# Optimization experiments

Measured on AMD Instinct MI355X. Metric: run time of the kernel, lower is better.

## Reference

```python
import jax, jax.numpy as jnp
import numpy as np

NUM_HEADS = 8


def setup_inputs() -> dict:
    key = jax.random.key(0)
    k0, k1, k2 = jax.random.split(key, 3)
    B, C, D, H, W = 2, 256, 16, 16, 8
    x = jax.random.normal(k0, (B, C, D, H, W), dtype=jnp.float32)
    # 1x1x1 Conv3d weights are pointwise linear maps over channels
    w_qkv = jax.random.normal(k1, (3 * C, C), dtype=jnp.float32) * 0.02
    b_qkv = jnp.zeros((3 * C,), dtype=jnp.float32)
    w_out = jax.random.normal(k2, (C, C), dtype=jnp.float32) * 0.02
    b_out = jnp.zeros((C,), dtype=jnp.float32)
    return {"x": x, "w_qkv": w_qkv, "b_qkv": b_qkv, "w_out": w_out, "b_out": b_out}


def reference(x, w_qkv, b_qkv, w_out, b_out):
    b, c, d, h, w = x.shape
    nh = NUM_HEADS
    hd = c // nh
    scale = hd ** (-0.5)
    n = d * h * w
    xf = x.reshape(b, c, n)  # flatten spatial volume to N tokens
    # to_qkv: pointwise conv == channel-mixing matmul
    qkv = jnp.einsum('oc,bcn->bon', w_qkv, xf) + b_qkv[None, :, None]
    # torch: view(b, H, 3*hd, N) then chunk(3, dim=2) -> per-head channel grouping
    qkv = qkv.reshape(b, nh, 3 * hd, n)
    q, k, v = jnp.split(qkv, 3, axis=2)  # each (b, nh, hd, n)
    sim = jnp.einsum('bhcn,bhcm->bhnm', q, k) * scale  # (b, nh, N, N)
    attn = jax.nn.softmax(sim, axis=-1)
    out = jnp.einsum('bhnm,bhcm->bhcn', attn, v)  # (b, nh, hd, N)
    out = out.reshape(b, c, n)
    out = jnp.einsum('oc,bcn->bon', w_out, out) + b_out[None, :, None]
    return x + out.reshape(b, c, d, h, w)
```

## Files before the change

kernel.cpp:

```cpp
#include <hip/hip_runtime.h>
#include <hip/hip_bf16.h>
#include <math.h>

#define BB 2
#define CC 256
#define NH 8
#define HD 32
#define NN 2048
#define QBLK 64
#define QK_SCALE 0.25500917f

typedef __attribute__((ext_vector_type(8))) short short8;
typedef __attribute__((ext_vector_type(8))) unsigned short ushort8;
typedef __attribute__((ext_vector_type(4))) float f32x4;

__device__ inline unsigned short f2bf(float f) {
    __hip_bfloat16 h = __float2bfloat16(f);
    return __builtin_bit_cast(unsigned short, h);
}
__device__ inline int xcd_chunk(int orig, int nwg) {
    int q = nwg >> 3, r = nwg & 7, x = orig & 7, s = orig >> 3;
    return (x < r ? x * (q + 1) : r * (q + 1) + (x - r) * q) + s;
}

__global__ __launch_bounds__(256) void qkv_mfma(const float* __restrict__ x,
                                                const float* __restrict__ wq,
                                                const float* __restrict__ bias,
                                                unsigned short* __restrict__ qt,
                                                unsigned short* __restrict__ ktt,
                                                unsigned short* __restrict__ vt) {
    const int l = xcd_chunk(blockIdx.x, 768);
    const int m0 = (l % 12) * 64;
    const int xtile = l / 12;
    const int n0 = (xtile & 31) * 64;
    const int b = xtile >> 5;
    const int t = threadIdx.x, lane = t & 63, wid = t >> 6;
    const int g = lane >> 4, ln = lane & 15;
    __shared__ __align__(16) unsigned short Aw[4][64][36];
    __shared__ __align__(16) unsigned short Bx[4][64][36];
    f32x4 acc[4] = {};

    const int sm = t & 63, sch = t >> 6;
    const int pc = t >> 4, pn = t & 15;
    const int c0 = pc * 8, nl = pn * 4;
    const float* xb = x + (size_t)b * CC * NN + n0;

    for (int kh = 0; kh < 2; ++kh) {
        __syncthreads();
        {
            const float* wsrc = wq + (size_t)(m0 + sm) * CC + kh * 128 + sch * 32;
            float wv[32];
#pragma unroll
            for (int j = 0; j < 8; ++j) *(float4*)&wv[j * 4] = *(const float4*)&wsrc[j * 4];
#pragma unroll
            for (int j2 = 0; j2 < 4; ++j2) {
                ushort8 p;
#pragma unroll
                for (int e = 0; e < 8; ++e) p[e] = f2bf(wv[j2 * 8 + e]);
                *(ushort8*)&Aw[sch][sm][j2 * 8] = p;
            }
        }
        {
            const float* xsrc = xb + (size_t)(kh * 128 + c0) * NN + nl;
            float xv[8][4];
#pragma unroll
            for (int i = 0; i < 8; ++i) *(float4*)&xv[i][0] = *(const float4*)&xsrc[(size_t)i * NN];
#pragma unroll
            for (int i2 = 0; i2 < 4; ++i2) {
                ushort8 p;
#pragma unroll
                for (int e = 0; e < 8; ++e) p[e] = f2bf(xv[e][i2]);
                *(ushort8*)&Bx[pc >> 2][nl + i2][(pc & 3) * 8] = p;
            }
        }
        __syncthreads();
#pragma unroll
        for (int ks = 0; ks < 4; ++ks) {
            short8 aW = *(const short8*)&Aw[ks][wid * 16 + ln][g * 8];
#pragma unroll
            for (int nt = 0; nt < 4; ++nt) {
                short8 bX = *(const short8*)&Bx[ks][nt * 16 + ln][g * 8];
                acc[nt] = __builtin_amdgcn_mfma_f32_16x16x32_bf16(aW, bX, acc[nt], 0, 0, 0);
            }
        }
    }
    __syncthreads();
    unsigned short (*Tqk)[64][40] = (unsigned short (*)[64][40])&Aw[0][0][0];
    unsigned short (*Tv)[32][72]  = (unsigned short (*)[32][72])&Bx[0][0][0];
    {
        const int grp = wid >> 1;
        const int cl0 = (wid & 1) * 16 + 4 * g;
        const int gm0 = m0 + grp * 32;
        const int gtype = (gm0 % 96) >> 5;
        const float sc = (gtype == 0) ? QK_SCALE : 1.0f;
        float bv[4];
#pragma unroll
        for (int r = 0; r < 4; ++r) bv[r] = bias[gm0 + cl0 + r];
        if (gtype == 2) {
#pragma unroll
            for (int nt = 0; nt < 4; ++nt)
#pragma unroll
                for (int r = 0; r < 4; ++r)
                    Tv[grp][cl0 + r][nt * 16 + ln] = f2bf(acc[nt][r] + bv[r]);
        } else {
#pragma unroll
            for (int nt = 0; nt < 4; ++nt)
#pragma unroll
                for (int r = 0; r < 4; ++r)
                    Tqk[grp][nt * 16 + ln][cl0 + r] = f2bf((acc[nt][r] + bv[r]) * sc);
        }
    }
    __syncthreads();
#pragma unroll
    for (int grp2 = 0; grp2 < 2; ++grp2) {
        const int gm = m0 + grp2 * 32;
        const int gtype = (gm % 96) >> 5;
        const int head = gm / 96;
        if (gtype == 2) {
            const int cl = t >> 3, n8 = (t & 7) * 8;
            ushort8 v = *(const ushort8*)&Tv[grp2][cl][n8];
            *(ushort8*)&vt[((size_t)(b * NH + head) * HD + cl) * NN + n0 + n8] = v;
        } else {
            unsigned short* dst = (gtype == 0) ? qt : ktt;
            const int nr = t >> 2, c8 = (t & 3) * 8;
            ushort8 v = *(const ushort8*)&Tqk[grp2][nr][c8];
            *(ushort8*)&dst[((size_t)(b * NH + head) * NN + n0 + nr) * HD + c8] = v;
        }
    }
}

__global__ __launch_bounds__(512, 4) void attn_mfma(const unsigned short* __restrict__ Qt,
                                                    const unsigned short* __restrict__ Kt,
                                                    const unsigned short* __restrict__ Vt,
                                                    unsigned short* __restrict__ aout_t) {
    const int l = xcd_chunk(blockIdx.x, 512);
    const int n0 = (l & 31) * QBLK;
    const int bh = l >> 5;
    const int h = bh & 7, b = bh >> 3;
    const int t = threadIdx.x;
    const int lane = t & 63, w = t >> 6;
    const int g = lane >> 4, ln = lane & 15;

    __shared__ float Of[8][64][18];
    __shared__ float Ls[8][64];

    const unsigned short* qb = Qt + ((size_t)(b * NH + h) * NN + n0) * HD;
    const unsigned short* kb = Kt + (size_t)(b * NH + h) * NN * HD;
    const unsigned short* vb = Vt + (size_t)(b * NH + h) * HD * NN;

    short8 bQ[4];
#pragma unroll
    for (int qt = 0; qt < 4; ++qt)
        bQ[qt] = *(const short8*)&qb[(size_t)(qt * 16 + ln) * HD + g * 8];

    const int krow = 8 * (ln >> 2) + (ln & 3);
    const int wkey0 = w * 256;

    f32x4 oacc[4][2];
    const f32x4 zero4 = {0.f, 0.f, 0.f, 0.f};
#pragma unroll
    for (int qt = 0; qt < 4; ++qt) { oacc[qt][0] = zero4; oacc[qt][1] = zero4; }
    float l_run[4] = {0.f, 0.f, 0.f, 0.f};

    short8 kA0 = *(const short8*)&kb[(size_t)(wkey0 + krow + 0) * HD + g * 8];
    short8 kA1 = *(const short8*)&kb[(size_t)(wkey0 + krow + 4) * HD + g * 8];

    for (int it = 0; it < 8; ++it) {
        const int kt0 = wkey0 + it * 32;
        short8 bV0 = *(const short8*)&vb[(size_t)ln * NN + kt0 + g * 8];
        short8 bV1 = *(const short8*)&vb[(size_t)(16 + ln) * NN + kt0 + g * 8];

        f32x4 sacc[2][4];
        __builtin_amdgcn_s_setprio(1);
#pragma unroll
        for (int qt = 0; qt < 4; ++qt) {
            sacc[0][qt] = __builtin_amdgcn_mfma_f32_16x16x32_bf16(kA0, bQ[qt], zero4, 0, 0, 0);
            sacc[1][qt] = __builtin_amdgcn_mfma_f32_16x16x32_bf16(kA1, bQ[qt], zero4, 0, 0, 0);
        }
        __builtin_amdgcn_s_setprio(0);

        if (it + 1 < 8) {
            kA0 = *(const short8*)&kb[(size_t)(kt0 + 32 + krow + 0) * HD + g * 8];
            kA1 = *(const short8*)&kb[(size_t)(kt0 + 32 + krow + 4) * HD + g * 8];
        }

        short8 aP[4];
#pragma unroll
        for (int qt = 0; qt < 4; ++qt) {
#pragma unroll
            for (int u = 0; u < 2; ++u) {
#pragma unroll
                for (int r = 0; r < 4; ++r) {
                    float p = exp2f(sacc[u][qt][r]);
                    sacc[u][qt][r] = p;
                    aP[qt][u * 4 + r] = (short)f2bf(p);
                }
            }
            l_run[qt] += ((sacc[0][qt][0] + sacc[0][qt][1]) + (sacc[0][qt][2] + sacc[0][qt][3]))
                       + ((sacc[1][qt][0] + sacc[1][qt][1]) + (sacc[1][qt][2] + sacc[1][qt][3]));
        }

        __builtin_amdgcn_s_setprio(1);
#pragma unroll
        for (int qt = 0; qt < 4; ++qt) {
            oacc[qt][0] = __builtin_amdgcn_mfma_f32_16x16x32_bf16(aP[qt], bV0, oacc[qt][0], 0, 0, 0);
            oacc[qt][1] = __builtin_amdgcn_mfma_f32_16x16x32_bf16(aP[qt], bV1, oacc[qt][1], 0, 0, 0);
        }
        __builtin_amdgcn_s_setprio(0);
    }

#pragma unroll
    for (int qt = 0; qt < 4; ++qt) {
        l_run[qt] += __shfl_xor(l_run[qt], 16);
        l_run[qt] += __shfl_xor(l_run[qt], 32);
    }

    const int rq = t >> 3, c2 = (t & 7) * 2;
    float linv = 0.f;
#pragma unroll
    for (int ch = 0; ch < 2; ++ch) {
        if (ch) __syncthreads();
#pragma unroll
        for (int qt = 0; qt < 4; ++qt)
#pragma unroll
            for (int r = 0; r < 4; ++r)
                Of[w][qt * 16 + 4 * g + r][ln] = oacc[qt][ch][r];
        if (ch == 0 && g == 0)
#pragma unroll
            for (int qt = 0; qt < 4; ++qt) Ls[w][qt * 16 + ln] = l_run[qt];
        __syncthreads();
        float s0 = 0.f, s1 = 0.f;
#pragma unroll
        for (int ww = 0; ww < 8; ++ww) {
            s0 += Of[ww][rq][c2];
            s1 += Of[ww][rq][c2 + 1];
        }
        if (ch == 0) {
            float lsum = 0.f;
#pragma unroll
            for (int ww = 0; ww < 8; ++ww) lsum += Ls[ww][rq];
            linv = 1.0f / lsum;
        }
        ushort2 r2;
        r2.x = f2bf(s0 * linv);
        r2.y = f2bf(s1 * linv);
        *(ushort2*)&aout_t[((size_t)b * NN + n0 + rq) * CC + h * HD + ch * 16 + c2] = r2;
    }
}

__global__ __launch_bounds__(256) void proj_mfma(const unsigned short* __restrict__ aout_t,
                                                 const float* __restrict__ wo,
                                                 const float* __restrict__ bias,
                                                 const float* __restrict__ x,
                                                 float* __restrict__ out) {
    const int l = xcd_chunk(blockIdx.x, 512);
    const int n0 = (l & 63) * 32;
    const int bm = l >> 6;
    const int m0 = (bm & 3) * 64, b = bm >> 2;
    const int t = threadIdx.x, lane = t & 63, wid = t >> 6;
    const int g = lane >> 4, ln = lane & 15;
    __shared__ __align__(16) unsigned short Aw[4][64][36];
    __shared__ __align__(16) unsigned short Bx[4][32][36];
    f32x4 acc[2] = {};
    const unsigned short* ab = aout_t + ((size_t)b * NN + n0) * CC;

    const int sm = t & 63, sch = t >> 6;
    const int bn = t & 31, bch = t >> 5;
    for (int kh = 0; kh < 2; ++kh) {
        __syncthreads();
        {
            const float* wsrc = wo + (size_t)(m0 + sm) * CC + kh * 128 + sch * 32;
            float wv[32];
#pragma unroll
            for (int j = 0; j < 8; ++j) *(float4*)&wv[j * 4] = *(const float4*)&wsrc[j * 4];
#pragma unroll
            for (int j2 = 0; j2 < 4; ++j2) {
                ushort8 p;
#pragma unroll
                for (int e = 0; e < 8; ++e) p[e] = f2bf(wv[j2 * 8 + e]);
                *(ushort8*)&Aw[sch][sm][j2 * 8] = p;
            }
        }
        {
            int ks = bch >> 1, off = (bch & 1) * 16;
            const unsigned short* src = &ab[(size_t)bn * CC + kh * 128 + ks * 32 + off];
            *(ushort8*)&Bx[ks][bn][off]     = *(const ushort8*)&src[0];
            *(ushort8*)&Bx[ks][bn][off + 8] = *(const ushort8*)&src[8];
        }
        __syncthreads();
#pragma unroll
        for (int ks = 0; ks < 4; ++ks) {
            short8 aW = *(const short8*)&Aw[ks][wid * 16 + ln][g * 8];
#pragma unroll
            for (int nt = 0; nt < 2; ++nt) {
                short8 bX = *(const short8*)&Bx[ks][nt * 16 + ln][g * 8];
                acc[nt] = __builtin_amdgcn_mfma_f32_16x16x32_bf16(aW, bX, acc[nt], 0, 0, 0);
            }
        }
    }
    const int mbase = m0 + wid * 16 + 4 * g;
    float bv[4];
#pragma unroll
    for (int r = 0; r < 4; ++r) bv[r] = bias[mbase + r];
#pragma unroll
    for (int nt = 0; nt < 2; ++nt) {
        int n = n0 + nt * 16 + ln;
#pragma unroll
        for (int r = 0; r < 4; ++r) {
            size_t off = ((size_t)b * CC + mbase + r) * NN + n;
            out[off] = acc[nt][r] + bv[r] + x[off];
        }
    }
}

extern "C" void kernel_launch(void* const* d_in, const int* in_sizes, int n_in,
                              void* d_out, int out_size, void* d_ws, size_t ws_size,
                              hipStream_t stream) {
    const float* x     = (const float*)d_in[0];
    const float* w_qkv = (const float*)d_in[1];
    const float* b_qkv = (const float*)d_in[2];
    const float* w_out = (const float*)d_in[3];
    const float* b_out = (const float*)d_in[4];
    float* out = (float*)d_out;

    unsigned short* qt     = (unsigned short*)d_ws;
    unsigned short* ktt    = qt  + (size_t)BB * NH * NN * HD;
    unsigned short* vt     = ktt + (size_t)BB * NH * NN * HD;
    unsigned short* aout_t = vt  + (size_t)BB * NH * NN * HD;

    qkv_mfma<<<dim3(768), 256, 0, stream>>>(x, w_qkv, b_qkv, qt, ktt, vt);
    attn_mfma<<<dim3(512), 512, 0, stream>>>(qt, ktt, vt, aout_t);
    proj_mfma<<<dim3(512), 256, 0, stream>>>(aout_t, w_out, b_out, x, out);
}
```

Measured before the change: 46.49 us.

## Fuse QKV, attention and projection into one cooperative persistent kernel

Merges the three separate launches into a single cooperative kernel of 512 blocks × 512 threads, with grid-wide syncs between the QKV projection, attention and output projection phases. The QKV phase is remapped to 512 threads over two passes of the 768 tiles, and the projection phase idles half the threads. The goal is to remove the launch gaps between kernels. In exchange it pays for two grid barriers, loses occupancy in the GEMM phases, and falls back to the three-kernel path if the cooperative launch fails.

```diff
diff --git a/kernel.cpp b/kernel.cpp
--- a/kernel.cpp
+++ b/kernel.cpp
@@ -1,6 +1,9 @@
 #include <hip/hip_runtime.h>
+#include <hip/hip_cooperative_groups.h>
 #include <hip/hip_bf16.h>
 #include <math.h>
+
+namespace cg = cooperative_groups;
 
 #define BB 2
 #define CC 256
@@ -21,6 +24,313 @@
 __device__ inline int xcd_chunk(int orig, int nwg) {
     int q = nwg >> 3, r = nwg & 7, x = orig & 7, s = orig >> 3;
     return (x < r ? x * (q + 1) : r * (q + 1) + (x - r) * q) + s;
+}
+
+__global__ __launch_bounds__(512, 4) void fused_spatial_attn(
+        const float* __restrict__ x,
+        const float* __restrict__ wq,
+        const float* __restrict__ bq,
+        const float* __restrict__ wo,
+        const float* __restrict__ bo,
+        unsigned short* __restrict__ qt,
+        unsigned short* __restrict__ ktt,
+        unsigned short* __restrict__ vt,
+        unsigned short* __restrict__ aout_t,
+        float* __restrict__ out) {
+    __shared__ __align__(16) unsigned char smem[38912];
+    const int t = threadIdx.x;
+    const int bid = blockIdx.x;
+    const int lane = t & 63, wid = t >> 6;
+    const int g = lane >> 4, ln = lane & 15;
+
+    {
+        auto Aw = (unsigned short (*)[64][36])smem;
+        auto Bx = (unsigned short (*)[64][36])(smem + 18432);
+        const int wm = wid & 3, wn = wid >> 2;
+        const int sm = t & 63, sc = t >> 6;
+        const int ksA = sc >> 1, offA = (sc & 1) * 16;
+        const int c0 = (t >> 4) * 4, nl = (t & 15) * 4;
+
+        for (int pass = 0; pass < 2; ++pass) {
+            const int slot = bid + pass * 512;
+            const bool act = (pass == 0) || (bid < 256);
+            const int m0 = (slot % 12) * 64;
+            const int xtile = slot / 12;
+            const int n0 = (xtile & 31) * 64;
+            const int b = (xtile >> 5) & 1;
+            const float* xb = x + (size_t)b * CC * NN + n0;
+            f32x4 acc[2] = {};
+
+            for (int kh = 0; kh < 2; ++kh) {
+                __syncthreads();
+                if (act) {
+                    {
+                        const float* wsrc = wq + (size_t)(m0 + sm) * CC + kh * 128 + sc * 16;
+                        float wv[16];
+#pragma unroll
+                        for (int j = 0; j < 4; ++j) *(float4*)&wv[j * 4] = *(const float4*)&wsrc[j * 4];
+                        ushort8 p0, p1;
+#pragma unroll
+                        for (int e = 0; e < 8; ++e) { p0[e] = f2bf(wv[e]); p1[e] = f2bf(wv[8 + e]); }
+                        *(ushort8*)&Aw[ksA][sm][offA] = p0;
+                        *(ushort8*)&Aw[ksA][sm][offA + 8] = p1;
+                    }
+                    {
+                        const float* xsrc = xb + (size_t)(kh * 128 + c0) * NN + nl;
+                        float xv[4][4];
+#pragma unroll
+                        for (int i = 0; i < 4; ++i) *(float4*)&xv[i][0] = *(const float4*)&xsrc[(size_t)i * NN];
+#pragma unroll
+                        for (int i2 = 0; i2 < 4; ++i2) {
+                            ushort4 p;
+                            p.x = f2bf(xv[0][i2]); p.y = f2bf(xv[1][i2]);
+                            p.z = f2bf(xv[2][i2]); p.w = f2bf(xv[3][i2]);
+                            *(ushort4*)&Bx[c0 >> 5][nl + i2][c0 & 31] = p;
+                        }
+                    }
+                }
+                __syncthreads();
+                if (act) {
+#pragma unroll
+                    for (int ks = 0; ks < 4; ++ks) {
+                        short8 aW = *(const short8*)&Aw[ks][wm * 16 + ln][g * 8];
+#pragma unroll
+                        for (int ntl = 0; ntl < 2; ++ntl) {
+                            short8 bX = *(const short8*)&Bx[ks][(wn * 2 + ntl) * 16 + ln][g * 8];
+                            acc[ntl] = __builtin_amdgcn_mfma_f32_16x16x32_bf16(aW, bX, acc[ntl], 0, 0, 0);
+                        }
+                    }
+                }
+            }
+            __syncthreads();
+            auto Tqk = (unsigned short (*)[64][40])smem;
+            auto Tv  = (unsigned short (*)[32][72])(smem + 18432);
+            if (act) {
+                const int grp = wm >> 1;
+                const int cl0 = (wm & 1) * 16 + 4 * g;
+                const int gm0 = m0 + grp * 32;
+                const int gtype = (gm0 % 96) >> 5;
+                const float sc2 = (gtype == 0) ? QK_SCALE : 1.0f;
+                float bv[4];
+#pragma unroll
+                for (int r = 0; r < 4; ++r) bv[r] = bq[gm0 + cl0 + r];
+                if (gtype == 2) {
+#pragma unroll
+                    for (int ntl = 0; ntl < 2; ++ntl)
+#pragma unroll
+                        for (int r = 0; r < 4; ++r)
+                            Tv[grp][cl0 + r][(wn * 2 + ntl) * 16 + ln] = f2bf(acc[ntl][r] + bv[r]);
+                } else {
+#pragma unroll
+                    for (int ntl = 0; ntl < 2; ++ntl)
+#pragma unroll
+                        for (int r = 0; r < 4; ++r)
+                            Tqk[grp][(wn * 2 + ntl) * 16 + ln][cl0 + r] = f2bf((acc[ntl][r] + bv[r]) * sc2);
+                }
+            }
+            __syncthreads();
+            if (act) {
+#pragma unroll
+                for (int grp2 = 0; grp2 < 2; ++grp2) {
+                    const int gm = m0 + grp2 * 32;
+                    const int gtype = (gm % 96) >> 5;
+                    const int head = gm / 96;
+                    if (gtype == 2) {
+                        const int cl = t >> 4, n4 = (t & 15) * 4;
+                        ushort4 v = *(const ushort4*)&Tv[grp2][cl][n4];
+                        *(ushort4*)&vt[((size_t)(b * NH + head) * HD + cl) * NN + n0 + n4] = v;
+                    } else {
+                        unsigned short* dst = (gtype == 0) ? qt : ktt;
+                        const int nr = t >> 3, c4 = (t & 7) * 4;
+                        ushort4 v = *(const ushort4*)&Tqk[grp2][nr][c4];
+                        *(ushort4*)&dst[((size_t)(b * NH + head) * NN + n0 + nr) * HD + c4] = v;
+                    }
+                }
+            }
+        }
+    }
+
+    cg::this_grid().sync();
+
+    {
+        const int n0 = (bid & 31) * QBLK;
+        const int bh = bid >> 5;
+        const int h = bh & 7, b = bh >> 3;
+        const int w = wid;
+
+        auto Of = (float (*)[64][18])smem;
+        auto Ls = (float (*)[64])(smem + 36864);
+
+        const unsigned short* qb = qt + ((size_t)(b * NH + h) * NN + n0) * HD;
+        const unsigned short* kb = ktt + (size_t)(b * NH + h) * NN * HD;
+        const unsigned short* vb = vt + (size_t)(b * NH + h) * HD * NN;
+
+        short8 bQ[4];
+#pragma unroll
+        for (int qt4 = 0; qt4 < 4; ++qt4)
+            bQ[qt4] = *(const short8*)&qb[(size_t)(qt4 * 16 + ln) * HD + g * 8];
+
+        const int krow = 8 * (ln >> 2) + (ln & 3);
+        const int wkey0 = w * 256;
+
+        f32x4 oacc[4][2];
+        const f32x4 zero4 = {0.f, 0.f, 0.f, 0.f};
+#pragma unroll
+        for (int qt4 = 0; qt4 < 4; ++qt4) { oacc[qt4][0] = zero4; oacc[qt4][1] = zero4; }
+        float l_run[4] = {0.f, 0.f, 0.f, 0.f};
+
+        short8 kA0 = *(const short8*)&kb[(size_t)(wkey0 + krow + 0) * HD + g * 8];
+        short8 kA1 = *(const short8*)&kb[(size_t)(wkey0 + krow + 4) * HD + g * 8];
+
+        for (int it = 0; it < 8; ++it) {
+            const int kt0 = wkey0 + it * 32;
+            short8 bV0 = *(const short8*)&vb[(size_t)ln * NN + kt0 + g * 8];
+            short8 bV1 = *(const short8*)&vb[(size_t)(16 + ln) * NN + kt0 + g * 8];
+
+            f32x4 sacc[2][4];
+            __builtin_amdgcn_s_setprio(1);
+#pragma unroll
+            for (int qt4 = 0; qt4 < 4; ++qt4) {
+                sacc[0][qt4] = __builtin_amdgcn_mfma_f32_16x16x32_bf16(kA0, bQ[qt4], zero4, 0, 0, 0);
+                sacc[1][qt4] = __builtin_amdgcn_mfma_f32_16x16x32_bf16(kA1, bQ[qt4], zero4, 0, 0, 0);
+            }
+            __builtin_amdgcn_s_setprio(0);
+
+            if (it + 1 < 8) {
+                kA0 = *(const short8*)&kb[(size_t)(kt0 + 32 + krow + 0) * HD + g * 8];
+                kA1 = *(const short8*)&kb[(size_t)(kt0 + 32 + krow + 4) * HD + g * 8];
+            }
+
+            short8 aP[4];
+#pragma unroll
+            for (int qt4 = 0; qt4 < 4; ++qt4) {
+#pragma unroll
+                for (int u = 0; u < 2; ++u) {
+#pragma unroll
+                    for (int r = 0; r < 4; ++r) {
+                        float p = exp2f(sacc[u][qt4][r]);
+                        sacc[u][qt4][r] = p;
+                        aP[qt4][u * 4 + r] = (short)f2bf(p);
+                    }
+                }
+                l_run[qt4] += ((sacc[0][qt4][0] + sacc[0][qt4][1]) + (sacc[0][qt4][2] + sacc[0][qt4][3]))
+                            + ((sacc[1][qt4][0] + sacc[1][qt4][1]) + (sacc[1][qt4][2] + sacc[1][qt4][3]));
+            }
+
+            __builtin_amdgcn_s_setprio(1);
+#pragma unroll
+            for (int qt4 = 0; qt4 < 4; ++qt4) {
+                oacc[qt4][0] = __builtin_amdgcn_mfma_f32_16x16x32_bf16(aP[qt4], bV0, oacc[qt4][0], 0, 0, 0);
+                oacc[qt4][1] = __builtin_amdgcn_mfma_f32_16x16x32_bf16(aP[qt4], bV1, oacc[qt4][1], 0, 0, 0);
+            }
+            __builtin_amdgcn_s_setprio(0);
+        }
+
+#pragma unroll
+        for (int qt4 = 0; qt4 < 4; ++qt4) {
+            l_run[qt4] += __shfl_xor(l_run[qt4], 16);
+            l_run[qt4] += __shfl_xor(l_run[qt4], 32);
+        }
+
+        const int rq = t >> 3, c2 = (t & 7) * 2;
+        float linv = 0.f;
+#pragma unroll
+        for (int ch = 0; ch < 2; ++ch) {
+            __syncthreads();
+#pragma unroll
+            for (int qt4 = 0; qt4 < 4; ++qt4)
+#pragma unroll
+                for (int r = 0; r < 4; ++r)
+                    Of[w][qt4 * 16 + 4 * g + r][ln] = oacc[qt4][ch][r];
+            if (ch == 0 && g == 0)
+#pragma unroll
+                for (int qt4 = 0; qt4 < 4; ++qt4) Ls[w][qt4 * 16 + ln] = l_run[qt4];
+            __syncthreads();
+            float s0 = 0.f, s1 = 0.f;
+#pragma unroll
+            for (int ww = 0; ww < 8; ++ww) {
+                s0 += Of[ww][rq][c2];
+                s1 += Of[ww][rq][c2 + 1];
+            }
+            if (ch == 0) {
+                float lsum = 0.f;
+#pragma unroll
+                for (int ww = 0; ww < 8; ++ww) lsum += Ls[ww][rq];
+                linv = 1.0f / lsum;
+            }
+            ushort2 r2;
+            r2.x = f2bf(s0 * linv);
+            r2.y = f2bf(s1 * linv);
+            *(ushort2*)&aout_t[((size_t)b * NN + n0 + rq) * CC + h * HD + ch * 16 + c2] = r2;
+        }
+    }
+
+    cg::this_grid().sync();
+
+    {
+        const int n0 = (bid & 63) * 32;
+        const int bm = bid >> 6;
+        const int m0 = (bm & 3) * 64, b = bm >> 2;
+        const bool act = (t < 256);
+        auto Aw = (unsigned short (*)[64][36])smem;
+        auto Bx = (unsigned short (*)[32][36])(smem + 18432);
+        f32x4 acc[2] = {};
+        const unsigned short* ab = aout_t + ((size_t)b * NN + n0) * CC;
+
+        const int sm = t & 63, sch = t >> 6;
+        const int bn = t & 31, bch = t >> 5;
+        for (int kh = 0; kh < 2; ++kh) {
+            __syncthreads();
+            if (act) {
+                {
+                    const float* wsrc = wo + (size_t)(m0 + sm) * CC + kh * 128 + sch * 32;
+                    float wv[32];
+#pragma unroll
+                    for (int j = 0; j < 8; ++j) *(float4*)&wv[j * 4] = *(const float4*)&wsrc[j * 4];
+#pragma unroll
+                    for (int j2 = 0; j2 < 4; ++j2) {
+                        ushort8 p;
+#pragma unroll
+                        for (int e = 0; e < 8; ++e) p[e] = f2bf(wv[j2 * 8 + e]);
+                        *(ushort8*)&Aw[sch][sm][j2 * 8] = p;
+                    }
+                }
+                {
+                    int ks = bch >> 1, off = (bch & 1) * 16;
+                    const unsigned short* src = &ab[(size_t)bn * CC + kh * 128 + ks * 32 + off];
+                    *(ushort8*)&Bx[ks][bn][off]     = *(const ushort8*)&src[0];
+                    *(ushort8*)&Bx[ks][bn][off + 8] = *(const ushort8*)&src[8];
+                }
+            }
+            __syncthreads();
+            if (act) {
+#pragma unroll
+                for (int ks = 0; ks < 4; ++ks) {
+                    short8 aW = *(const short8*)&Aw[ks][wid * 16 + ln][g * 8];
+#pragma unroll
+                    for (int nt = 0; nt < 2; ++nt) {
+                        short8 bX = *(const short8*)&Bx[ks][nt * 16 + ln][g * 8];
+                        acc[nt] = __builtin_amdgcn_mfma_f32_16x16x32_bf16(aW, bX, acc[nt], 0, 0, 0);
+                    }
+                }
+            }
+        }
+        if (act) {
+            const int mbase = m0 + wid * 16 + 4 * g;
+            float bv[4];
+#pragma unroll
+            for (int r = 0; r < 4; ++r) bv[r] = bo[mbase + r];
+#pragma unroll
+            for (int nt = 0; nt < 2; ++nt) {
+                int n = n0 + nt * 16 + ln;
+#pragma unroll
+                for (int r = 0; r < 4; ++r) {
+                    size_t off = ((size_t)b * CC + mbase + r) * NN + n;
+                    out[off] = acc[nt][r] + bv[r] + x[off];
+                }
+            }
+        }
+    }
 }
 
 __global__ __launch_bounds__(256) void qkv_mfma(const float* __restrict__ x,
@@ -39,12 +349,10 @@
     __shared__ __align__(16) unsigned short Aw[4][64][36];
     __shared__ __align__(16) unsigned short Bx[4][64][36];
     f32x4 acc[4] = {};
-
     const int sm = t & 63, sch = t >> 6;
     const int pc = t >> 4, pn = t & 15;
     const int c0 = pc * 8, nl = pn * 4;
     const float* xb = x + (size_t)b * CC * NN + n0;
-
     for (int kh = 0; kh < 2; ++kh) {
         __syncthreads();
         {
@@ -140,94 +448,81 @@
     const int t = threadIdx.x;
     const int lane = t & 63, w = t >> 6;
     const int g = lane >> 4, ln = lane & 15;
-
     __shared__ float Of[8][64][18];
     __shared__ float Ls[8][64];
-
     const unsigned short* qb = Qt + ((size_t)(b * NH + h) * NN + n0) * HD;
     const unsigned short* kb = Kt + (size_t)(b * NH + h) * NN * HD;
     const unsigned short* vb = Vt + (size_t)(b * NH + h) * HD * NN;
-
     short8 bQ[4];
 #pragma unroll
-    for (int qt = 0; qt < 4; ++qt)
-        bQ[qt] = *(const short8*)&qb[(size_t)(qt * 16 + ln) * HD + g * 8];
-
+    for (int qt4 = 0; qt4 < 4; ++qt4)
+        bQ[qt4] = *(const short8*)&qb[(size_t)(qt4 * 16 + ln) * HD + g * 8];
     const int krow = 8 * (ln >> 2) + (ln & 3);
     const int wkey0 = w * 256;
-
     f32x4 oacc[4][2];
     const f32x4 zero4 = {0.f, 0.f, 0.f, 0.f};
 #pragma unroll
-    for (int qt = 0; qt < 4; ++qt) { oacc[qt][0] = zero4; oacc[qt][1] = zero4; }
+    for (int qt4 = 0; qt4 < 4; ++qt4) { oacc[qt4][0] = zero4; oacc[qt4][1] = zero4; }
     float l_run[4] = {0.f, 0.f, 0.f, 0.f};
-
     short8 kA0 = *(const short8*)&kb[(size_t)(wkey0 + krow + 0) * HD + g * 8];
     short8 kA1 = *(const short8*)&kb[(size_t)(wkey0 + krow + 4) * HD + g * 8];
-
     for (int it = 0; it < 8; ++it) {
         const int kt0 = wkey0 + it * 32;
         short8 bV0 = *(const short8*)&vb[(size_t)ln * NN + kt0 + g * 8];
         short8 bV1 = *(const short8*)&vb[(size_t)(16 + ln) * NN + kt0 + g * 8];
-
         f32x4 sacc[2][4];
         __builtin_amdgcn_s_setprio(1);
 #pragma unroll
-        for (int qt = 0; qt < 4; ++qt) {
-            sacc[0][qt] = __builtin_amdgcn_mfma_f32_16x16x32_bf16(kA0, bQ[qt], zero4, 0, 0, 0);
-            sacc[1][qt] = __builtin_amdgcn_mfma_f32_16x16x32_bf16(kA1, bQ[qt], zero4, 0, 0, 0);
+        for (int qt4 = 0; qt4 < 4; ++qt4) {
+            sacc[0][qt4] = __builtin_amdgcn_mfma_f32_16x16x32_bf16(kA0, bQ[qt4], zero4, 0, 0, 0);
+            sacc[1][qt4] = __builtin_amdgcn_mfma_f32_16x16x32_bf16(kA1, bQ[qt4], zero4, 0, 0, 0);
         }
         __builtin_amdgcn_s_setprio(0);
-
         if (it + 1 < 8) {
             kA0 = *(const short8*)&kb[(size_t)(kt0 + 32 + krow + 0) * HD + g * 8];
             kA1 = *(const short8*)&kb[(size_t)(kt0 + 32 + krow + 4) * HD + g * 8];
         }
-
         short8 aP[4];
 #pragma unroll
-        for (int qt = 0; qt < 4; ++qt) {
+        for (int qt4 = 0; qt4 < 4; ++qt4) {
 #pragma unroll
             for (int u = 0; u < 2; ++u) {
 #pragma unroll
                 for (int r = 0; r < 4; ++r) {
-                    float p = exp2f(sacc[u][qt][r]);
-                    sacc[u][qt][r] = p;
-                    aP[qt][u * 4 + r] = (short)f2bf(p);
-                }
-            }
-            l_run[qt] += ((sacc[0][qt][0] + sacc[0][qt][1]) + (sacc[0][qt][2] + sacc[0][qt][3]))
-                       + ((sacc[1][qt][0] + sacc[1][qt][1]) + (sacc[1][qt][2] + sacc[1][qt][3]));
-        }
-
+                    float p = exp2f(sacc[u][qt4][r]);
+                    sacc[u][qt4][r] = p;
+                    aP[qt4][u * 4 + r] = (short)f2bf(p);
+                }
+            }
+            l_run[qt4] += ((sacc[0][qt4][0] + sacc[0][qt4][1]) + (sacc[0][qt4][2] + sacc[0][qt4][3]))
+                        + ((sacc[1][qt4][0] + sacc[1][qt4][1]) + (sacc[1][qt4][2] + sacc[1][qt4][3]));
+        }
         __builtin_amdgcn_s_setprio(1);
 #pragma unroll
-        for (int qt = 0; qt < 4; ++qt) {
-            oacc[qt][0] = __builtin_amdgcn_mfma_f32_16x16x32_bf16(aP[qt], bV0, oacc[qt][0], 0, 0, 0);
-            oacc[qt][1] = __builtin_amdgcn_mfma_f32_16x16x32_bf16(aP[qt], bV1, oacc[qt][1], 0, 0, 0);
+        for (int qt4 = 0; qt4 < 4; ++qt4) {
+            oacc[qt4][0] = __builtin_amdgcn_mfma_f32_16x16x32_bf16(aP[qt4], bV0, oacc[qt4][0], 0, 0, 0);
+            oacc[qt4][1] = __builtin_amdgcn_mfma_f32_16x16x32_bf16(aP[qt4], bV1, oacc[qt4][1], 0, 0, 0);
         }
         __builtin_amdgcn_s_setprio(0);
     }
-
-#pragma unroll
-    for (int qt = 0; qt < 4; ++qt) {
-        l_run[qt] += __shfl_xor(l_run[qt], 16);
-        l_run[qt] += __shfl_xor(l_run[qt], 32);
-    }
-
+#pragma unroll
+    for (int qt4 = 0; qt4 < 4; ++qt4) {
+        l_run[qt4] += __shfl_xor(l_run[qt4], 16);
+        l_run[qt4] += __shfl_xor(l_run[qt4], 32);
+    }
     const int rq = t >> 3, c2 = (t & 7) * 2;
     float linv = 0.f;
 #pragma unroll
     for (int ch = 0; ch < 2; ++ch) {
-        if (ch) __syncthreads();
-#pragma unroll
-        for (int qt = 0; qt < 4; ++qt)
+        __syncthreads();
+#pragma unroll
+        for (int qt4 = 0; qt4 < 4; ++qt4)
 #pragma unroll
             for (int r = 0; r < 4; ++r)
-                Of[w][qt * 16 + 4 * g + r][ln] = oacc[qt][ch][r];
+                Of[w][qt4 * 16 + 4 * g + r][ln] = oacc[qt4][ch][r];
         if (ch == 0 && g == 0)
 #pragma unroll
-            for (int qt = 0; qt < 4; ++qt) Ls[w][qt * 16 + ln] = l_run[qt];
+            for (int qt4 = 0; qt4 < 4; ++qt4) Ls[w][qt4 * 16 + ln] = l_run[qt4];
         __syncthreads();
         float s0 = 0.f, s1 = 0.f;
 #pragma unroll
@@ -263,7 +558,6 @@
     __shared__ __align__(16) unsigned short Bx[4][32][36];
     f32x4 acc[2] = {};
     const unsigned short* ab = aout_t + ((size_t)b * NN + n0) * CC;
-
     const int sm = t & 63, sch = t >> 6;
     const int bn = t & 31, bch = t >> 5;
     for (int kh = 0; kh < 2; ++kh) {
@@ -328,7 +622,14 @@
     unsigned short* vt     = ktt + (size_t)BB * NH * NN * HD;
     unsigned short* aout_t = vt  + (size_t)BB * NH * NN * HD;
 
-    qkv_mfma<<<dim3(768), 256, 0, stream>>>(x, w_qkv, b_qkv, qt, ktt, vt);
-    attn_mfma<<<dim3(512), 512, 0, stream>>>(qt, ktt, vt, aout_t);
-    proj_mfma<<<dim3(512), 256, 0, stream>>>(aout_t, w_out, b_out, x, out);
+    void* args[] = {(void*)&x, (void*)&w_qkv, (void*)&b_qkv, (void*)&w_out, (void*)&b_out,
+                    (void*)&qt, (void*)&ktt, (void*)&vt, (void*)&aout_t, (void*)&out};
+    hipError_t err = hipLaunchCooperativeKernel((void*)fused_spatial_attn, dim3(512),
+                                                dim3(512), args, 0, stream);
+    if (err != hipSuccess) {
+        (void)hipGetLastError();
+        qkv_mfma<<<dim3(768), 256, 0, stream>>>(x, w_qkv, b_qkv, qt, ktt, vt);
+        attn_mfma<<<dim3(512), 512, 0, stream>>>(qt, ktt, vt, aout_t);
+        proj_mfma<<<dim3(512), 256, 0, stream>>>(aout_t, w_out, b_out, x, out);
+    }
 }
```

New measurement: 173.4 us. +272.9%, slower.
